# Performance work log

Measured on AMD Instinct MI355X. Metric: run time of the kernel, lower is better.

The kernel has to match this reference:

```python
import jax, jax.numpy as jnp
import numpy as np

N_QUBITS = 6
N_LAYERS = 6
DIM = 2 ** N_QUBITS  # 64


def _qft_matrix():
    # PennyLane qml.QFT matrix: F[j,k] = exp(2*pi*i*j*k/N) / sqrt(N)
    j = np.arange(DIM)
    F = np.exp(2j * np.pi * np.outer(j, j) / DIM) / np.sqrt(DIM)
    return jnp.asarray(F, dtype=jnp.complex64)


def _cnot_ring_perm():
    # Composite permutation of basis states for CNOT(q, (q+1)%n) applied q=0..n-1.
    # Wire 0 is the most significant bit (PennyLane convention).
    m = np.arange(DIM)
    for q in range(N_QUBITS):
        c_bit = N_QUBITS - 1 - q
        t_bit = N_QUBITS - 1 - ((q + 1) % N_QUBITS)
        ctrl = (m >> c_bit) & 1
        m = np.where(ctrl == 1, m ^ (1 << t_bit), m)
    # state_out[m_final] = state_in[m_init]  ->  gather index = argsort(m)
    return jnp.asarray(np.argsort(m), dtype=jnp.int32)


_QFT = _qft_matrix()
_CNOT_PERM = _cnot_ring_perm()


def _layer_unitary(thetas):
    # kron of per-qubit RY(theta) gates (they act on distinct wires -> single 64x64 matrix)
    c = jnp.cos(thetas / 2.0)
    s = jnp.sin(thetas / 2.0)
    U = jnp.array(1.0, dtype=thetas.dtype).reshape(1, 1)
    for q in range(N_QUBITS):
        g = jnp.stack([jnp.stack([c[q], -s[q]]), jnp.stack([s[q], c[q]])])  # [2,2]
        U = jnp.kron(U, g)
    return U.astype(jnp.complex64)  # [64,64]


def setup_inputs() -> dict:
    key = jax.random.key(0)
    k1, k2 = jax.random.split(key)
    x = jax.random.normal(k1, (65536, DIM), dtype=jnp.float32)
    weights_rot = jax.random.normal(k2, (N_LAYERS, N_QUBITS), dtype=jnp.float32) * 0.01
    return {"x": x, "weights_rot": weights_rot}


def reference(x, weights_rot):
    # AmplitudeEmbedding with normalize=True
    norm = jnp.sqrt(jnp.sum(x * x, axis=-1, keepdims=True))
    psi = (x / norm).astype(jnp.complex64)  # [B, 64]
    # QFT on all wires
    psi = jnp.einsum('jk,bk->bj', _QFT, psi)
    # layers: fused RY-on-all-wires unitary, then CNOT ring permutation
    for l in range(N_LAYERS):
        U = _layer_unitary(weights_rot[l])
        psi = jnp.einsum('ij,bj->bi', U, psi)
        psi = jnp.take(psi, _CNOT_PERM, axis=1)
    # probs over all wires
    return psi.real ** 2 + psi.imag ** 2  # [B, 64] float32
```

## Files before the change

kernel.cpp:

```cpp
#include <hip/hip_runtime.h>
#include <hip/hip_bf16.h>

#define NQ 6
#define DIM 64
#define NLAYERS 6

typedef __attribute__((ext_vector_type(8))) short bf16x8;
typedef __attribute__((ext_vector_type(4))) float f32x4;

#define GLOAD_LDS16(gp, lp) \
    __builtin_amdgcn_global_load_lds((const __attribute__((address_space(1))) void*)(gp), \
                                     (__attribute__((address_space(3))) void*)(lp), 16, 0, 0)

__global__ __launch_bounds__(64) void build_M(const float* __restrict__ w,
                                              unsigned short* __restrict__ Bf) {
    const int k = blockIdx.x;
    const int j = threadIdx.x;

    int t = (j * k) & 63;
    float sv, cv;
    __sincosf((float)t * (3.14159265358979f / 32.0f), &sv, &cv);
    float vr = cv * 0.125f;
    float vi = sv * 0.125f;

    int m = j;
#pragma unroll
    for (int q = 0; q < NQ; ++q) {
        int cb = 5 - q;
        int tb = 5 - ((q + 1) % NQ);
        if ((m >> cb) & 1) m ^= (1 << tb);
    }
    const int dst4 = m << 2;

#pragma unroll
    for (int l = 0; l < NLAYERS; ++l) {
#pragma unroll
        for (int q = 0; q < NQ; ++q) {
            float th = w[l * NQ + q] * 0.5f;
            float c = __cosf(th), s = __sinf(th);
            int b = 5 - q;
            float pr = __shfl_xor(vr, 1 << b);
            float pi = __shfl_xor(vi, 1 << b);
            float sgn = ((j >> b) & 1) ? s : -s;
            vr = c * vr + sgn * pr;
            vi = c * vi + sgn * pi;
        }
        vr = __int_as_float(__builtin_amdgcn_ds_permute(dst4, __float_as_int(vr)));
        vi = __int_as_float(__builtin_amdgcn_ds_permute(dst4, __float_as_int(vi)));
    }

    const int jt = j >> 4;
    const int lane16 = (j & 15) + 16 * ((k >> 3) & 3);
    const int chunk = k >> 5;
    const int e = k & 7;
    const int base = ((jt * 2 + chunk) * 2) * 512 + lane16 * 8 + e;

    __hip_bfloat16 rh = __float2bfloat16(vr);
    __hip_bfloat16 ih = __float2bfloat16(vi);
    Bf[base]       = *(unsigned short*)&rh;
    Bf[base + 512] = *(unsigned short*)&ih;
}

__device__ __forceinline__ void split8(const float* f, bf16x8& h, bf16x8& l) {
#pragma unroll
    for (int i = 0; i < 8; ++i) {
        __hip_bfloat16 hh = __float2bfloat16(f[i]);
        __hip_bfloat16 ll = __float2bfloat16(f[i] - __bfloat162float(hh));
        h[i] = *(short*)&hh;
        l[i] = *(short*)&ll;
    }
}

__global__ __launch_bounds__(512) void qenc_main(const float* __restrict__ x,
                                                 const unsigned short* __restrict__ Bf,
                                                 float* __restrict__ out) {
    __shared__ __align__(16) unsigned short sB[8192];
    const int tid = threadIdx.x;
    const int lane = tid & 63;
    const int wid = tid >> 6;
    const int row0 = blockIdx.x * 128 + wid * 16;
    const int r = lane & 15;
    const int g = lane >> 4;

    const float* xp = x + (size_t)(row0 + r) * DIM + 8 * g;
    float4 va = *(const float4*)(xp);
    float4 vb = *(const float4*)(xp + 4);
    float4 vc = *(const float4*)(xp + 32);
    float4 vd = *(const float4*)(xp + 36);

    {
        const unsigned short* gp = Bf + (size_t)tid * 8;
        unsigned short* lp = sB + (size_t)tid * 8;
        GLOAD_LDS16(gp, lp);
        GLOAD_LDS16(gp + 4096, lp + 4096);
    }

    float xf[16];
    *(float4*)(xf)      = va;  *(float4*)(xf + 4)  = vb;
    *(float4*)(xf + 8)  = vc;  *(float4*)(xf + 12) = vd;

    float n0 = 0.f;
#pragma unroll
    for (int i = 0; i < 16; ++i) n0 = fmaf(xf[i], xf[i], n0);
    n0 += __shfl_xor(n0, 16);
    n0 += __shfl_xor(n0, 32);
    const float inv = 1.0f / n0;

    bf16x8 xh[2], xl[2];
    split8(xf,     xh[0], xl[0]);
    split8(xf + 8, xh[1], xl[1]);

    __syncthreads();

    const f32x4 z = {0.f, 0.f, 0.f, 0.f};
    f32x4 acr[4] = {z, z, z, z};
    f32x4 aci[4] = {z, z, z, z};
    const unsigned short* bp = sB + lane * 8;

#pragma unroll
    for (int jt = 0; jt < 4; ++jt) {
#pragma unroll
        for (int c = 0; c < 2; ++c) {
            const unsigned short* fb = bp + ((jt * 2 + c) * 2) * 512;
            bf16x8 mr = *(const bf16x8*)(fb);
            bf16x8 mi = *(const bf16x8*)(fb + 512);
            acr[jt] = __builtin_amdgcn_mfma_f32_16x16x32_bf16(mr, xh[c], acr[jt], 0, 0, 0);
            acr[jt] = __builtin_amdgcn_mfma_f32_16x16x32_bf16(mr, xl[c], acr[jt], 0, 0, 0);
            aci[jt] = __builtin_amdgcn_mfma_f32_16x16x32_bf16(mi, xh[c], aci[jt], 0, 0, 0);
            aci[jt] = __builtin_amdgcn_mfma_f32_16x16x32_bf16(mi, xl[c], aci[jt], 0, 0, 0);
        }
    }

    float* op = out + (size_t)(row0 + r) * DIM + 4 * g;
#pragma unroll
    for (int jt = 0; jt < 4; ++jt) {
        float4 o;
        o.x = (acr[jt][0] * acr[jt][0] + aci[jt][0] * aci[jt][0]) * inv;
        o.y = (acr[jt][1] * acr[jt][1] + aci[jt][1] * aci[jt][1]) * inv;
        o.z = (acr[jt][2] * acr[jt][2] + aci[jt][2] * aci[jt][2]) * inv;
        o.w = (acr[jt][3] * acr[jt][3] + aci[jt][3] * aci[jt][3]) * inv;
        *(float4*)(op + jt * 16) = o;
    }
}

extern "C" void kernel_launch(void* const* d_in, const int* in_sizes, int n_in,
                              void* d_out, int out_size, void* d_ws, size_t ws_size,
                              hipStream_t stream) {
    const float* x = (const float*)d_in[0];
    const float* w = (const float*)d_in[1];
    float* out = (float*)d_out;
    unsigned short* Bf = (unsigned short*)d_ws;
    int B = in_sizes[0] / DIM;

    hipLaunchKernelGGL(build_M, dim3(DIM), dim3(64), 0, stream, w, Bf);
    hipLaunchKernelGGL(qenc_main, dim3(B / 128), dim3(512), 0, stream, x, Bf, out);
}
```

Measured before the change: 17.82 us.

## Fuse unitary construction into main kernel, recomputing matrix per block in LDS

```diff
diff --git a/kernel.cpp b/kernel.cpp
--- a/kernel.cpp
+++ b/kernel.cpp
@@ -8,72 +8,9 @@
 typedef __attribute__((ext_vector_type(8))) short bf16x8;
 typedef __attribute__((ext_vector_type(4))) float f32x4;
 
-#define GLOAD_LDS16(gp, lp) \
-    __builtin_amdgcn_global_load_lds((const __attribute__((address_space(1))) void*)(gp), \
-                                     (__attribute__((address_space(3))) void*)(lp), 16, 0, 0)
-
-__global__ __launch_bounds__(64) void build_M(const float* __restrict__ w,
-                                              unsigned short* __restrict__ Bf) {
-    const int k = blockIdx.x;
-    const int j = threadIdx.x;
-
-    int t = (j * k) & 63;
-    float sv, cv;
-    __sincosf((float)t * (3.14159265358979f / 32.0f), &sv, &cv);
-    float vr = cv * 0.125f;
-    float vi = sv * 0.125f;
-
-    int m = j;
-#pragma unroll
-    for (int q = 0; q < NQ; ++q) {
-        int cb = 5 - q;
-        int tb = 5 - ((q + 1) % NQ);
-        if ((m >> cb) & 1) m ^= (1 << tb);
-    }
-    const int dst4 = m << 2;
-
-#pragma unroll
-    for (int l = 0; l < NLAYERS; ++l) {
-#pragma unroll
-        for (int q = 0; q < NQ; ++q) {
-            float th = w[l * NQ + q] * 0.5f;
-            float c = __cosf(th), s = __sinf(th);
-            int b = 5 - q;
-            float pr = __shfl_xor(vr, 1 << b);
-            float pi = __shfl_xor(vi, 1 << b);
-            float sgn = ((j >> b) & 1) ? s : -s;
-            vr = c * vr + sgn * pr;
-            vi = c * vi + sgn * pi;
-        }
-        vr = __int_as_float(__builtin_amdgcn_ds_permute(dst4, __float_as_int(vr)));
-        vi = __int_as_float(__builtin_amdgcn_ds_permute(dst4, __float_as_int(vi)));
-    }
-
-    const int jt = j >> 4;
-    const int lane16 = (j & 15) + 16 * ((k >> 3) & 3);
-    const int chunk = k >> 5;
-    const int e = k & 7;
-    const int base = ((jt * 2 + chunk) * 2) * 512 + lane16 * 8 + e;
-
-    __hip_bfloat16 rh = __float2bfloat16(vr);
-    __hip_bfloat16 ih = __float2bfloat16(vi);
-    Bf[base]       = *(unsigned short*)&rh;
-    Bf[base + 512] = *(unsigned short*)&ih;
-}
-
-__device__ __forceinline__ void split8(const float* f, bf16x8& h, bf16x8& l) {
-#pragma unroll
-    for (int i = 0; i < 8; ++i) {
-        __hip_bfloat16 hh = __float2bfloat16(f[i]);
-        __hip_bfloat16 ll = __float2bfloat16(f[i] - __bfloat162float(hh));
-        h[i] = *(short*)&hh;
-        l[i] = *(short*)&ll;
-    }
-}
-
-__global__ __launch_bounds__(512) void qenc_main(const float* __restrict__ x,
-                                                 const unsigned short* __restrict__ Bf,
-                                                 float* __restrict__ out) {
+__global__ __launch_bounds__(512, 4) void qenc_fused(const float* __restrict__ x,
+                                                     const float* __restrict__ w,
+                                                     float* __restrict__ out) {
     __shared__ __align__(16) unsigned short sB[8192];
     const int tid = threadIdx.x;
     const int lane = tid & 63;
@@ -88,11 +25,68 @@
     float4 vc = *(const float4*)(xp + 32);
     float4 vd = *(const float4*)(xp + 36);
 
+    const int j = lane;
+    float vr[8], vi[8];
+#pragma unroll
+    for (int c8 = 0; c8 < 8; ++c8) {
+        int k = wid * 8 + c8;
+        int t = (j * k) & 63;
+        float sv, cv;
+        __sincosf((float)t * (3.14159265358979f / 32.0f), &sv, &cv);
+        vr[c8] = cv * 0.125f;
+        vi[c8] = sv * 0.125f;
+    }
+
+    int m = j;
+#pragma unroll
+    for (int q = 0; q < NQ; ++q) {
+        int cb = 5 - q;
+        int tb = 5 - ((q + 1) % NQ);
+        if ((m >> cb) & 1) m ^= (1 << tb);
+    }
+    const int dst4 = m << 2;
+
+#pragma unroll
+    for (int l = 0; l < NLAYERS; ++l) {
+        float cc[NQ], ss[NQ];
+#pragma unroll
+        for (int q = 0; q < NQ; ++q) {
+            float th = w[l * NQ + q] * 0.5f;
+            cc[q] = __cosf(th);
+            ss[q] = __sinf(th);
+        }
+#pragma unroll
+        for (int q = 0; q < NQ; ++q) {
+            int b = 5 - q;
+            float sgn = ((j >> b) & 1) ? ss[q] : -ss[q];
+#pragma unroll
+            for (int c8 = 0; c8 < 8; ++c8) {
+                float pr = __shfl_xor(vr[c8], 1 << b);
+                float pi = __shfl_xor(vi[c8], 1 << b);
+                vr[c8] = cc[q] * vr[c8] + sgn * pr;
+                vi[c8] = cc[q] * vi[c8] + sgn * pi;
+            }
+        }
+#pragma unroll
+        for (int c8 = 0; c8 < 8; ++c8) {
+            vr[c8] = __int_as_float(__builtin_amdgcn_ds_permute(dst4, __float_as_int(vr[c8])));
+            vi[c8] = __int_as_float(__builtin_amdgcn_ds_permute(dst4, __float_as_int(vi[c8])));
+        }
+    }
+
+    bf16x8 regR, regI;
+#pragma unroll
+    for (int c8 = 0; c8 < 8; ++c8) {
+        __hip_bfloat16 rh = __float2bfloat16(vr[c8]);
+        __hip_bfloat16 ih = __float2bfloat16(vi[c8]);
+        regR[c8] = *(short*)&rh;
+        regI[c8] = *(short*)&ih;
+    }
     {
-        const unsigned short* gp = Bf + (size_t)tid * 8;
-        unsigned short* lp = sB + (size_t)tid * 8;
-        GLOAD_LDS16(gp, lp);
-        GLOAD_LDS16(gp + 4096, lp + 4096);
+        const int jt = j >> 4;
+        const int fbase = ((jt * 2 + (wid >> 2)) * 2) * 512 + ((j & 15) + 16 * (wid & 3)) * 8;
+        *(bf16x8*)(sB + fbase)       = regR;
+        *(bf16x8*)(sB + fbase + 512) = regI;
     }
 
     float xf[16];
@@ -107,8 +101,16 @@
     const float inv = 1.0f / n0;
 
     bf16x8 xh[2], xl[2];
-    split8(xf,     xh[0], xl[0]);
-    split8(xf + 8, xh[1], xl[1]);
+#pragma unroll
+    for (int c = 0; c < 2; ++c)
+#pragma unroll
+        for (int i = 0; i < 8; ++i) {
+            float f = xf[c * 8 + i];
+            __hip_bfloat16 hh = __float2bfloat16(f);
+            __hip_bfloat16 ll = __float2bfloat16(f - __bfloat162float(hh));
+            xh[c][i] = *(short*)&hh;
+            xl[c][i] = *(short*)&ll;
+        }
 
     __syncthreads();
 
@@ -149,9 +151,7 @@
     const float* x = (const float*)d_in[0];
     const float* w = (const float*)d_in[1];
     float* out = (float*)d_out;
-    unsigned short* Bf = (unsigned short*)d_ws;
     int B = in_sizes[0] / DIM;
 
-    hipLaunchKernelGGL(build_M, dim3(DIM), dim3(64), 0, stream, w, Bf);
-    hipLaunchKernelGGL(qenc_main, dim3(B / 128), dim3(512), 0, stream, x, Bf, out);
+    hipLaunchKernelGGL(qenc_fused, dim3(B / 128), dim3(512), 0, stream, x, w, out);
 }
```

Measured after the change: 39.88 us. 2.24x slower.
